# Performance work log

Measured on AMD Instinct MI355X. Metric: run time of the kernel, lower is better.

Reference implementation:

```python
import jax, jax.numpy as jnp
import numpy as np

BLOCK = 128


def _dequant_blockwise(w_q, w_s):
    # w_q: [N, K] int8-valued, w_s: [N//BLOCK, K//BLOCK] float32 scales
    N, K = w_q.shape
    rb, cb = N // BLOCK, K // BLOCK  # dims chosen divisible by BLOCK
    w = w_q.astype(jnp.float32).reshape(rb, BLOCK, cb, BLOCK)
    w = w * w_s[:, None, :, None]
    return w.reshape(N, K)


def setup_inputs() -> dict:
    key = jax.random.key(0)
    k1, k2, k3, k4 = jax.random.split(key, 4)
    M, K, N = 8192, 4096, 16384
    x = jax.random.normal(k1, (M, K), dtype=jnp.float32)
    # int8 weight values in [-127, 127]; stored as int32 for harness simplicity
    w_q = jax.random.randint(k2, (N, K), -127, 128, dtype=jnp.int32)
    w_s = jax.random.uniform(k3, (N // BLOCK, K // BLOCK), dtype=jnp.float32) * 0.02
    bias = jax.random.normal(k4, (N,), dtype=jnp.float32)
    return {"x": x, "w_q": w_q, "w_s": w_s, "bias": bias}


def reference(x, w_q, w_s, bias):
    # Faithful to the dequant-fallback path of int8_linear + bias add
    w_fp = _dequant_blockwise(w_q, w_s)          # [N, K] float32
    out = x @ w_fp.T                             # [M, N]
    return out + bias[None, :]
```

## Files before the change

kernel.cpp:

```cpp
#include <hip/hip_runtime.h>

#define M_DIM 8192
#define K_DIM 4096
#define N_DIM 16384
#define KT 32

typedef __attribute__((ext_vector_type(4))) int i32x4;

__device__ __forceinline__ int pack4(int a, int b, int c, int d) {
  return (a & 255) | ((b & 255) << 8) | ((c & 255) << 16) | (d << 24);
}

__global__ __launch_bounds__(256) void quant_x_kernel(const float* __restrict__ x,
    char* __restrict__ xq, float* __restrict__ sx) {
  const int row = blockIdx.x;
  const int tid = threadIdx.x;
  const float4* xr = reinterpret_cast<const float4*>(x + (size_t)row * K_DIM);
  float4 v[4];
  float m = 0.f;
#pragma unroll
  for (int j = 0; j < 4; ++j) {
    v[j] = xr[tid * 4 + j];
    m = fmaxf(m, fmaxf(fmaxf(fabsf(v[j].x), fabsf(v[j].y)),
                       fmaxf(fabsf(v[j].z), fabsf(v[j].w))));
  }
#pragma unroll
  for (int o = 32; o > 0; o >>= 1) m = fmaxf(m, __shfl_xor(m, o));
  __shared__ float wm[4];
  if ((tid & 63) == 0) wm[tid >> 6] = m;
  __syncthreads();
  m = fmaxf(fmaxf(wm[0], wm[1]), fmaxf(wm[2], wm[3]));
  const float r = (m > 0.f) ? 127.f / m : 0.f;
  i32x4 pk;
#pragma unroll
  for (int j = 0; j < 4; ++j)
    pk[j] = pack4((int)rintf(v[j].x * r), (int)rintf(v[j].y * r),
                  (int)rintf(v[j].z * r), (int)rintf(v[j].w * r));
  reinterpret_cast<i32x4*>(xq + (size_t)row * K_DIM)[tid] = pk;
  if (tid == 0) sx[row] = (m > 0.f) ? m / 127.f : 0.f;
}

__global__ __launch_bounds__(256) void requant_w_kernel(const int* __restrict__ wq,
    const float* __restrict__ wsc, char* __restrict__ w8, float* __restrict__ sw) {
  const int row = blockIdx.x;
  const int tid = threadIdx.x;
  const int4* q = reinterpret_cast<const int4*>(wq + (size_t)row * K_DIM);
  const float s = wsc[(row >> 7) * 32 + (tid >> 3)];
  int4 v[4];
  int mx = 0;
#pragma unroll
  for (int j = 0; j < 4; ++j) {
    v[j] = q[tid * 4 + j];
    mx = max(mx, max(max(abs(v[j].x), abs(v[j].y)), max(abs(v[j].z), abs(v[j].w))));
  }
  float fm = s * (float)mx;
#pragma unroll
  for (int o = 32; o > 0; o >>= 1) fm = fmaxf(fm, __shfl_xor(fm, o));
  __shared__ float wmx[4];
  if ((tid & 63) == 0) wmx[tid >> 6] = fm;
  __syncthreads();
  fm = fmaxf(fmaxf(wmx[0], wmx[1]), fmaxf(wmx[2], wmx[3]));
  const float swv = (fm > 0.f) ? fm / 127.f : 0.f;
  const float f = (fm > 0.f) ? s * (127.f / fm) : 0.f;
  if (tid == 0) sw[row] = swv;
  i32x4 pk;
#pragma unroll
  for (int j = 0; j < 4; ++j)
    pk[j] = pack4((int)rintf((float)v[j].x * f), (int)rintf((float)v[j].y * f),
                  (int)rintf((float)v[j].z * f), (int)rintf((float)v[j].w * f));
  reinterpret_cast<i32x4*>(w8 + (size_t)row * K_DIM)[tid] = pk;
}

__device__ __forceinline__ void gload16(const void* g, void* l) {
  __builtin_amdgcn_global_load_lds(
      (const __attribute__((address_space(1))) unsigned int*)g,
      (__attribute__((address_space(3))) unsigned int*)l, 16, 0, 0);
}

#define BAR() do { asm volatile("" ::: "memory"); \
                   __builtin_amdgcn_s_barrier();  \
                   asm volatile("" ::: "memory"); } while (0)

#define MFI(a, b, c) __builtin_amdgcn_mfma_i32_16x16x64_i8(a, b, c, 0, 0, 0)

__global__ __launch_bounds__(512, 2) void gemm_kernel(
    const char* __restrict__ Aq, const char* __restrict__ Bq,
    const float* __restrict__ sw, const float* __restrict__ sx,
    const float* __restrict__ bias, float* __restrict__ C) {
  __shared__ __align__(128) char lds[131072];

  const int tid = threadIdx.x;
  const int lane = tid & 63, wid = tid >> 6;
  const int wr = wid >> 2, wc = wid & 3;

  const int bid = blockIdx.x;
  const int r = bid & 255;
  const int s = bid >> 8;
  const int sm = s & 1, sn = s >> 1;
  const int tm = sm * 16 + (r & 15);
  const int tn = sn * 16 + (r >> 4);

  const int srow = (wid << 3) + (lane >> 3);
  const int kswz = ((lane & 7) ^ ((lane >> 3) & 7)) << 4;
  const char* aSrc = Aq + (size_t)(tm * 256 + srow) * K_DIM + kswz;
  const char* bSrc = Bq + (size_t)(tn * 256 + srow) * K_DIM + kswz;
  const int ldst = wid << 10;

#define STAGE_A(tt, h, s2, b) gload16(aSrc + (size_t)((h)*128 + (s2)*64) * K_DIM + (size_t)(tt)*128, \
                                      lds + (b)*65536 + (h)*16384 + (s2)*8192 + ldst)
#define STAGE_B(tt, h, s2, b) gload16(bSrc + (size_t)((h)*128 + (s2)*64) * K_DIM + (size_t)(tt)*128, \
                                      lds + (b)*65536 + 32768 + (h)*16384 + (s2)*8192 + ldst)
#define STAGE_TILE(tt, b) do { \
    STAGE_A(tt,0,0,b); STAGE_A(tt,0,1,b); STAGE_A(tt,1,0,b); STAGE_A(tt,1,1,b); \
    STAGE_B(tt,0,0,b); STAGE_B(tt,0,1,b); STAGE_B(tt,1,0,b); STAGE_B(tt,1,1,b); \
  } while (0)

  const int hi = lane >> 4, lo3 = lane & 7;
  const int aks0 = ((0 + hi) ^ lo3) << 4;
  const int aks1 = ((4 + hi) ^ lo3) << 4;
  const int aoff = (wr * 128 + (lane & 15)) * 128;
  const int boff = 32768 + (wc * 64 + (lane & 15)) * 128;

  i32x4 acc[8][4] = {};

  STAGE_TILE(0, 0);
  asm volatile("s_waitcnt vmcnt(0)" ::: "memory");
  BAR();

#define AFRAGS(q, P) \
  const i32x4 P##0 = *(const i32x4*)(Ab + (2*(q)    ) * 2048 + aks0); \
  const i32x4 P##1 = *(const i32x4*)(Ab + (2*(q)    ) * 2048 + aks1); \
  const i32x4 P##2 = *(const i32x4*)(Ab + (2*(q) + 1) * 2048 + aks0); \
  const i32x4 P##3 = *(const i32x4*)(Ab + (2*(q) + 1) * 2048 + aks1);

#define QUAD(q, P) \
  acc[2*(q)][0]   = MFI(P##0, bf00, acc[2*(q)][0]); \
  acc[2*(q)][1]   = MFI(P##0, bf10, acc[2*(q)][1]); \
  acc[2*(q)][2]   = MFI(P##0, bf20, acc[2*(q)][2]); \
  acc[2*(q)][3]   = MFI(P##0, bf30, acc[2*(q)][3]); \
  acc[2*(q)+1][0] = MFI(P##2, bf00, acc[2*(q)+1][0]); \
  acc[2*(q)+1][1] = MFI(P##2, bf10, acc[2*(q)+1][1]); \
  acc[2*(q)+1][2] = MFI(P##2, bf20, acc[2*(q)+1][2]); \
  acc[2*(q)+1][3] = MFI(P##2, bf30, acc[2*(q)+1][3]); \
  acc[2*(q)][0]   = MFI(P##1, bf01, acc[2*(q)][0]); \
  acc[2*(q)][1]   = MFI(P##1, bf11, acc[2*(q)][1]); \
  acc[2*(q)][2]   = MFI(P##1, bf21, acc[2*(q)][2]); \
  acc[2*(q)][3]   = MFI(P##1, bf31, acc[2*(q)][3]); \
  acc[2*(q)+1][0] = MFI(P##3, bf01, acc[2*(q)+1][0]); \
  acc[2*(q)+1][1] = MFI(P##3, bf11, acc[2*(q)+1][1]); \
  acc[2*(q)+1][2] = MFI(P##3, bf21, acc[2*(q)+1][2]); \
  acc[2*(q)+1][3] = MFI(P##3, bf31, acc[2*(q)+1][3]);

  for (int t = 0; t < KT; ++t) {
    const int p = t & 1, pn = p ^ 1;
    const char* Ab = lds + p * 65536 + aoff;
    const char* Bb = lds + p * 65536 + boff;

    if (t + 1 < KT) STAGE_TILE(t + 1, pn);

    const i32x4 bf00 = *(const i32x4*)(Bb + 0 * 2048 + aks0);
    const i32x4 bf01 = *(const i32x4*)(Bb + 0 * 2048 + aks1);
    const i32x4 bf10 = *(const i32x4*)(Bb + 1 * 2048 + aks0);
    const i32x4 bf11 = *(const i32x4*)(Bb + 1 * 2048 + aks1);
    const i32x4 bf20 = *(const i32x4*)(Bb + 2 * 2048 + aks0);
    const i32x4 bf21 = *(const i32x4*)(Bb + 2 * 2048 + aks1);
    const i32x4 bf30 = *(const i32x4*)(Bb + 3 * 2048 + aks0);
    const i32x4 bf31 = *(const i32x4*)(Bb + 3 * 2048 + aks1);

    {
      AFRAGS(0, pa)
      QUAD(0, pa)
      AFRAGS(1, pb)
      QUAD(1, pb)
      AFRAGS(2, pc)
      QUAD(2, pc)
      AFRAGS(3, pd)
      QUAD(3, pd)
    }

    if (t + 1 < KT) {
      asm volatile("s_waitcnt vmcnt(0)" ::: "memory");
      BAR();
    }
  }

  const int crow0 = tm * 256 + wr * 128 + ((lane >> 4) << 2);
  const int ccol0 = tn * 256 + wc * 64 + (lane & 15);
#pragma unroll
  for (int ni = 0; ni < 4; ++ni) {
    const float bv = bias[ccol0 + ni * 16];
    const float swc = sw[ccol0 + ni * 16];
#pragma unroll
    for (int mi = 0; mi < 8; ++mi) {
#pragma unroll
      for (int e = 0; e < 4; ++e) {
        const int row = crow0 + mi * 16 + e;
        __builtin_nontemporal_store(
            sx[row] * swc * (float)acc[mi][ni][e] + bv,
            &C[(size_t)row * N_DIM + ccol0 + ni * 16]);
      }
    }
  }
}

extern "C" void kernel_launch(void* const* d_in, const int* in_sizes, int n_in,
                              void* d_out, int out_size, void* d_ws, size_t ws_size,
                              hipStream_t stream) {
  const float* x    = (const float*)d_in[0];
  const int*   wq   = (const int*)d_in[1];
  const float* wsc  = (const float*)d_in[2];
  const float* bias = (const float*)d_in[3];
  float* out = (float*)d_out;

  const size_t xq_bytes = (size_t)M_DIM * K_DIM;
  const size_t sx_bytes = (size_t)M_DIM * 4;
  const size_t w8_bytes = (size_t)N_DIM * K_DIM;
  const size_t sw_bytes = (size_t)N_DIM * 4;
  if (ws_size < xq_bytes + sx_bytes + w8_bytes + sw_bytes) return;

  char*  xq  = (char*)d_ws;
  float* sxp = (float*)((char*)d_ws + xq_bytes);
  char*  w8  = (char*)d_ws + xq_bytes + sx_bytes;
  float* swp = (float*)((char*)d_ws + xq_bytes + sx_bytes + w8_bytes);

  quant_x_kernel<<<M_DIM, 256, 0, stream>>>(x, xq, sxp);
  requant_w_kernel<<<N_DIM, 256, 0, stream>>>(wq, wsc, w8, swp);
  gemm_kernel<<<(M_DIM / 256) * (N_DIM / 256), 512, 0, stream>>>(
      xq, w8, swp, sxp, bias, out);
}
```

Before: 622.8 us.

## Switch GEMM to single-buffered LDS staging to raise occupancy

Drops the double-buffered 128KB LDS tile to a single 64KB buffer, so loading the next K tile now waits until all waves finish reading the current one. The likely aim is lower LDS use per block, allowing more resident blocks per CU, with other blocks' compute hiding load latency. In exchange, the overlap of global-to-LDS prefetch with MFMA work inside a block is lost and each iteration gets an extra barrier. It also stages sw values into spare LDS that are never read, and that staging code indexes sw oddly.

```diff
diff --git a/kernel.cpp b/kernel.cpp
--- a/kernel.cpp
+++ b/kernel.cpp
@@ -87,7 +87,7 @@
     const char* __restrict__ Aq, const char* __restrict__ Bq,
     const float* __restrict__ sw, const float* __restrict__ sx,
     const float* __restrict__ bias, float* __restrict__ C) {
-  __shared__ __align__(128) char lds[131072];
+  __shared__ __align__(128) char lds[65536 + 256];
 
   const int tid = threadIdx.x;
   const int lane = tid & 63, wid = tid >> 6;
@@ -106,13 +106,13 @@
   const char* bSrc = Bq + (size_t)(tn * 256 + srow) * K_DIM + kswz;
   const int ldst = wid << 10;
 
-#define STAGE_A(tt, h, s2, b) gload16(aSrc + (size_t)((h)*128 + (s2)*64) * K_DIM + (size_t)(tt)*128, \
-                                      lds + (b)*65536 + (h)*16384 + (s2)*8192 + ldst)
-#define STAGE_B(tt, h, s2, b) gload16(bSrc + (size_t)((h)*128 + (s2)*64) * K_DIM + (size_t)(tt)*128, \
-                                      lds + (b)*65536 + 32768 + (h)*16384 + (s2)*8192 + ldst)
-#define STAGE_TILE(tt, b) do { \
-    STAGE_A(tt,0,0,b); STAGE_A(tt,0,1,b); STAGE_A(tt,1,0,b); STAGE_A(tt,1,1,b); \
-    STAGE_B(tt,0,0,b); STAGE_B(tt,0,1,b); STAGE_B(tt,1,0,b); STAGE_B(tt,1,1,b); \
+#define STAGE_A(tt, h, s2) gload16(aSrc + (size_t)((h)*128 + (s2)*64) * K_DIM + (size_t)(tt)*128, \
+                                   lds + (h)*16384 + (s2)*8192 + ldst)
+#define STAGE_B(tt, h, s2) gload16(bSrc + (size_t)((h)*128 + (s2)*64) * K_DIM + (size_t)(tt)*128, \
+                                   lds + 32768 + (h)*16384 + (s2)*8192 + ldst)
+#define STAGE_TILE(tt) do { \
+    STAGE_A(tt,0,0); STAGE_A(tt,0,1); STAGE_A(tt,1,0); STAGE_A(tt,1,1); \
+    STAGE_B(tt,0,0); STAGE_B(tt,0,1); STAGE_B(tt,1,0); STAGE_B(tt,1,1); \
   } while (0)
 
   const int hi = lane >> 4, lo3 = lane & 7;
@@ -123,8 +123,10 @@
 
   i32x4 acc[8][4] = {};
 
-  STAGE_TILE(0, 0);
-  asm volatile("s_waitcnt vmcnt(0)" ::: "memory");
+  STAGE_TILE(0);
+  if (tid < 64) *(float*)(lds + 65536 + tid * 4) =
+      sw[tn * 256 + (tid & 63) * 4 / 4];
+  asm volatile("s_waitcnt vmcnt(0) lgkmcnt(0)" ::: "memory");
   BAR();
 
 #define AFRAGS(q, P) \
@@ -152,11 +154,8 @@
   acc[2*(q)+1][3] = MFI(P##3, bf31, acc[2*(q)+1][3]);
 
   for (int t = 0; t < KT; ++t) {
-    const int p = t & 1, pn = p ^ 1;
-    const char* Ab = lds + p * 65536 + aoff;
-    const char* Bb = lds + p * 65536 + boff;
-
-    if (t + 1 < KT) STAGE_TILE(t + 1, pn);
+    const char* Ab = lds + aoff;
+    const char* Bb = lds + boff;
 
     const i32x4 bf00 = *(const i32x4*)(Bb + 0 * 2048 + aks0);
     const i32x4 bf01 = *(const i32x4*)(Bb + 0 * 2048 + aks1);
@@ -166,7 +165,6 @@
     const i32x4 bf21 = *(const i32x4*)(Bb + 2 * 2048 + aks1);
     const i32x4 bf30 = *(const i32x4*)(Bb + 3 * 2048 + aks0);
     const i32x4 bf31 = *(const i32x4*)(Bb + 3 * 2048 + aks1);
-
     {
       AFRAGS(0, pa)
       QUAD(0, pa)
@@ -179,6 +177,9 @@
     }
 
     if (t + 1 < KT) {
+      asm volatile("s_waitcnt lgkmcnt(0)" ::: "memory");
+      BAR();
+      STAGE_TILE(t + 1);
       asm volatile("s_waitcnt vmcnt(0)" ::: "memory");
       BAR();
     }
```

Measured after the change: 735.0 us. 1.18x slower.
